# Kernel tuning notes

Measured on AMD Instinct MI355X. Metric: run time of the kernel, lower is better.

Reference implementation:

```python
import jax, jax.numpy as jnp
import numpy as np

B, N, D, S, ITERS = 64, 4096, 256, 8, 3
EPS = 1e-5


def _ln(x, g, b):
    m = jnp.mean(x, axis=-1, keepdims=True)
    v = jnp.mean((x - m) ** 2, axis=-1, keepdims=True)
    return (x - m) * jax.lax.rsqrt(v + EPS) * g + b


def setup_inputs() -> dict:
    key = jax.random.key(0)
    ks = jax.random.split(key, 20)
    s = 1.0 / np.sqrt(D)
    inp = {
        'x': jax.random.normal(ks[0], (B, N, D), jnp.float32),
        'noise': jax.random.normal(ks[1], (B, S, D), jnp.float32),
        'slot_mu': jax.random.normal(ks[2], (1, 1, D), jnp.float32),
        'slot_sigma': jax.random.normal(ks[3], (1, 1, D), jnp.float32) * 0.1,
        'Wq': jax.random.uniform(ks[4], (D, D), jnp.float32, -s, s),
        'bq': jnp.zeros((D,), jnp.float32),
        'Wk': jax.random.uniform(ks[5], (D, D), jnp.float32, -s, s),
        'bk': jnp.zeros((D,), jnp.float32),
        'Wv': jax.random.uniform(ks[6], (D, D), jnp.float32, -s, s),
        'bv': jnp.zeros((D,), jnp.float32),
        'W_ih': jax.random.uniform(ks[7], (3 * D, D), jnp.float32, -s, s),
        'b_ih': jnp.zeros((3 * D,), jnp.float32),
        'W_hh': jax.random.uniform(ks[8], (3 * D, D), jnp.float32, -s, s),
        'b_hh': jnp.zeros((3 * D,), jnp.float32),
        'W1': jax.random.uniform(ks[9], (D, D), jnp.float32, -s, s),
        'b1': jnp.zeros((D,), jnp.float32),
        'W2': jax.random.uniform(ks[10], (D, D), jnp.float32, -s, s),
        'b2': jnp.zeros((D,), jnp.float32),
        'g_in': jnp.ones((D,), jnp.float32), 'be_in': jnp.zeros((D,), jnp.float32),
        'g_sl': jnp.ones((D,), jnp.float32), 'be_sl': jnp.zeros((D,), jnp.float32),
        'g_mlp': jnp.ones((D,), jnp.float32), 'be_mlp': jnp.zeros((D,), jnp.float32),
    }
    return inp


def reference(x, noise, slot_mu, slot_sigma, Wq, bq, Wk, bk, Wv, bv,
              W_ih, b_ih, W_hh, b_hh, W1, b1, W2, b2,
              g_in, be_in, g_sl, be_sl, g_mlp, be_mlp):
    # slot init: mu + exp(sigma) * noise, broadcast over (B, S, D)
    slots = slot_mu + jnp.exp(slot_sigma) * noise

    xn = _ln(x, g_in, be_in)
    k = jnp.einsum('bnd,ed->bne', xn, Wk) + bk
    v = jnp.einsum('bnd,ed->bne', xn, Wv) + bv

    for _ in range(ITERS):
        sn = _ln(slots, g_sl, be_sl)
        q = jnp.einsum('bsd,ed->bse', sn, Wq) + bq
        attn_logits = jnp.einsum('bsd,bnd->bsn', q, k)
        attn = jax.nn.softmax(attn_logits, axis=-1)  # softmax over inputs N (as in source)
        updates = jnp.einsum('bnd,bsn->bsd', v, attn)

        # GRUCell: input=updates, hidden=slots (flattened over B*S)
        u = updates.reshape(-1, D)
        h = slots.reshape(-1, D)
        gx = u @ W_ih.T + b_ih
        gh = h @ W_hh.T + b_hh
        xr, xz, xn_g = jnp.split(gx, 3, axis=-1)
        hr, hz, hn_g = jnp.split(gh, 3, axis=-1)
        r = jax.nn.sigmoid(xr + hr)
        z = jax.nn.sigmoid(xz + hz)
        n = jnp.tanh(xn_g + r * hn_g)
        h = (1.0 - z) * n + z * h
        slots = h.reshape(x.shape[0], -1, D)

        m = _ln(slots, g_mlp, be_mlp)
        slots = slots + jax.nn.relu(m @ W1.T + b1) @ W2.T + b2
    return slots
```

## Files before the change

kernel.cpp:

```cpp
#include <hip/hip_runtime.h>

#define B_ 64
#define N_ 4096
#define D_ 256
#define S_ 8
#define EPSL 1e-5f

typedef _Float16 f16x8 __attribute__((ext_vector_type(8)));
typedef _Float16 f16x4 __attribute__((ext_vector_type(4)));
typedef float f32x4 __attribute__((ext_vector_type(4)));

__device__ __forceinline__ void gload_lds16_nt(const void* g, void* l){
    __builtin_amdgcn_global_load_lds(
        (const __attribute__((address_space(1))) unsigned int*)g,
        (__attribute__((address_space(3))) unsigned int*)l, 16, 0, 2);
}

__global__ __launch_bounds__(256) void k_ln_x(const float* __restrict__ x,
        const float* __restrict__ g, const float* __restrict__ be,
        _Float16* __restrict__ xn) {
    int w = threadIdx.x >> 6, l = threadIdx.x & 63;
    long row = (long)blockIdx.x * 4 + w;
    float4 xv = *(const float4*)(x + row * D_ + l * 4);
    float s = xv.x + xv.y + xv.z + xv.w;
    float q = xv.x*xv.x + xv.y*xv.y + xv.z*xv.z + xv.w*xv.w;
    #pragma unroll
    for (int m = 1; m < 64; m <<= 1) { s += __shfl_xor(s, m); q += __shfl_xor(q, m); }
    float mean = s * (1.0f/D_);
    float var = q * (1.0f/D_) - mean*mean;
    float inv = rsqrtf(var + EPSL);
    float4 gv = *(const float4*)(g + l*4);
    float4 bv = *(const float4*)(be + l*4);
    f16x4 o;
    o[0] = (_Float16)((xv.x-mean)*inv*gv.x + bv.x);
    o[1] = (_Float16)((xv.y-mean)*inv*gv.y + bv.y);
    o[2] = (_Float16)((xv.z-mean)*inv*gv.z + bv.z);
    o[3] = (_Float16)((xv.w-mean)*inv*gv.w + bv.w);
    *(f16x4*)(xn + row * D_ + l*4) = o;
}

__global__ __launch_bounds__(256) void k_wprep(const float* __restrict__ Whh,
        const float* __restrict__ W1, const float* __restrict__ W2,
        _Float16* __restrict__ Whhf, _Float16* __restrict__ W1f,
        _Float16* __restrict__ W2f) {
    int r = blockIdx.x, t = threadIdx.x;
    const float* src; _Float16* dst; int row;
    if (r < 768){ src = Whh; dst = Whhf; row = r; }
    else if (r < 1024){ src = W1; dst = W1f; row = r - 768; }
    else { src = W2; dst = W2f; row = r - 1024; }
    float v = src[(long)(r < 768 ? r : (r < 1024 ? r-768 : r-1024))*256 + t];
    long di = (long)((((row>>4)*8 + (t>>5))*64 + ((t>>3)&3)*16 + (row&15)))*8 + (t&7);
    dst[di] = (_Float16)v;
}

__global__ __launch_bounds__(256) void k_wprep2(const float* __restrict__ Wih,
        const float* __restrict__ Wv, const float* __restrict__ Wq,
        const float* __restrict__ Wk, const float* __restrict__ bih,
        const float* __restrict__ bv, const float* __restrict__ bq,
        _Float16* __restrict__ Wcf, _Float16* __restrict__ Wqkf,
        float* __restrict__ bc, float* __restrict__ cq) {
    __shared__ float a[4][256];
    int r = blockIdx.x, t = threadIdx.x;
    int w = t>>6, l = t&63;
    bool isC = (r < 192);
    if (isC){
        #pragma unroll
        for (int k=0;k<4;k++) a[k][t] = Wih[(long)(r*4+k)*256 + t];
    } else {
        int dbase = (r-192)*4;
        #pragma unroll
        for (int k=0;k<4;k++) a[k][t] = Wk[(long)t*256 + dbase + k];
    }
    __syncthreads();
    float ac[4] = {0.f,0.f,0.f,0.f};
    const float* Bm = isC ? Wv : Wq;
    for (int e=0;e<256;e++){
        float bvv = Bm[(long)e*256 + t];
        ac[0] += a[0][e]*bvv; ac[1] += a[1][e]*bvv;
        ac[2] += a[2][e]*bvv; ac[3] += a[3][e]*bvv;
    }
    _Float16* dst = isC ? Wcf : Wqkf;
    int rb = isC ? r*4 : (r-192)*4;
    #pragma unroll
    for (int k=0;k<4;k++){
        int row = rb + k;
        long di = (long)((((row>>4)*8 + (t>>5))*64 + ((t>>3)&3)*16 + (row&15)))*8 + (t&7);
        dst[di] = (_Float16)ac[k];
    }
    if (w < 4){
        const float* bvec = isC ? bv : bq;
        float p = 0.f;
        #pragma unroll
        for (int q=0;q<4;q++) p += a[w][l + q*64] * bvec[l + q*64];
        #pragma unroll
        for (int m=1;m<64;m<<=1) p += __shfl_xor(p, m);
        if (l==0){
            if (isC) bc[r*4 + w] = p + bih[r*4 + w];
            else     cq[(r-192)*4 + w] = p;
        }
    }
}

__device__ __forceinline__ void a16_st4(_Float16* a, int row, int col, float4 v){
    int byte = row*512 + ((col*2) ^ ((row&7)<<4));
    f16x4 h; h[0]=(_Float16)v.x; h[1]=(_Float16)v.y; h[2]=(_Float16)v.z; h[3]=(_Float16)v.w;
    *(f16x4*)((char*)a + byte) = h;
}
__device__ __forceinline__ void a16_st2(_Float16* a, int row, int col, _Float16 v){
    int byte = row*512 + ((col*2) ^ ((row&7)<<4));
    *(_Float16*)((char*)a + byte) = v;
}
__device__ __forceinline__ f16x8 a16_ld8(const _Float16* a, int row, int col){
    int byte = row*512 + ((col*2) ^ ((row&7)<<4));
    return *(const f16x8*)((const char*)a + byte);
}
__device__ __forceinline__ f16x8 wfrag_ld(const _Float16* __restrict__ Wf,
        int tt, int ks, int l){
    return *(const f16x8*)(Wf + ((long)tt*4096 + (ks*64 + l)*8));
}

template<int NT, int OS>
__device__ __forceinline__ void mm_stage_f(const _Float16* a16,
        const _Float16* __restrict__ Wf, float* outl, int w, int l){
    int lr = l&15, lh = l>>4;
    f16x8 A[8];
    #pragma unroll
    for (int ks=0;ks<8;ks++) A[ks] = a16_ld8(a16, lr, lh*8 + ks*32);
    #pragma unroll
    for (int tile=0; tile<NT; ++tile){
        int tt = w*NT + tile;
        f32x4 acc = {0.f,0.f,0.f,0.f};
        #pragma unroll
        for (int ks=0;ks<8;ks++)
            acc = __builtin_amdgcn_mfma_f32_16x16x32_f16(A[ks], wfrag_ld(Wf,tt,ks,l), acc, 0,0,0);
        if (lh < 2){
            #pragma unroll
            for (int r=0;r<4;r++) outl[(lh*4+r)*OS + tt*16 + lr] = acc[r];
        }
    }
}

__device__ __forceinline__ void mm_gates_f(const _Float16* au, const _Float16* ah,
        const _Float16* __restrict__ Wcf, const _Float16* __restrict__ Whf,
        float* g1, float* g2, int w, int l){
    int lr = l&15, lh = l>>4;
    f16x8 Au[8], Ah[8];
    #pragma unroll
    for (int ks=0;ks<8;ks++){ Au[ks] = a16_ld8(au, lr, lh*8+ks*32);
                              Ah[ks] = a16_ld8(ah, lr, lh*8+ks*32); }
    #pragma unroll
    for (int tile=0; tile<6; ++tile){
        int tt = w*6 + tile;
        f32x4 a1 = {0.f,0.f,0.f,0.f}, a2 = {0.f,0.f,0.f,0.f};
        #pragma unroll
        for (int ks=0;ks<8;ks++)
            a1 = __builtin_amdgcn_mfma_f32_16x16x32_f16(Au[ks], wfrag_ld(Wcf,tt,ks,l), a1, 0,0,0);
        #pragma unroll
        for (int ks=0;ks<8;ks++)
            a2 = __builtin_amdgcn_mfma_f32_16x16x32_f16(Ah[ks], wfrag_ld(Whf,tt,ks,l), a2, 0,0,0);
        if (lh < 2){
            #pragma unroll
            for (int r=0;r<4;r++){
                int s = lh*4+r;
                g1[s*768 + tt*16 + lr] = a1[r];
                g2[s*768 + tt*16 + lr] = a2[r];
            }
        }
    }
}

__global__ __launch_bounds__(512) void k_init(const float* __restrict__ noise,
        const float* __restrict__ mu, const float* __restrict__ sg,
        const float* __restrict__ g_sl, const float* __restrict__ be_sl,
        const _Float16* __restrict__ Wqkf, const float* __restrict__ cq,
        float* __restrict__ slots, _Float16* __restrict__ qh16) {
    __shared__ __align__(16) _Float16 a16[16*256];
    __shared__ float g1[8*256];
    int t = threadIdx.x, w = t>>6, l = t&63, b = blockIdx.x;
    int col = l*4;
    float4 nz = *(const float4*)(noise + ((long)b*8+w)*256 + col);
    float4 muv = *(const float4*)(mu + col);
    float4 sgv = *(const float4*)(sg + col);
    float4 sl;
    sl.x = muv.x + __expf(sgv.x)*nz.x; sl.y = muv.y + __expf(sgv.y)*nz.y;
    sl.z = muv.z + __expf(sgv.z)*nz.z; sl.w = muv.w + __expf(sgv.w)*nz.w;
    *(float4*)(slots + ((long)b*8+w)*256 + col) = sl;
    float s1 = sl.x+sl.y+sl.z+sl.w;
    float s2 = sl.x*sl.x+sl.y*sl.y+sl.z*sl.z+sl.w*sl.w;
    #pragma unroll
    for (int m=1;m<64;m<<=1){ s1+=__shfl_xor(s1,m); s2+=__shfl_xor(s2,m); }
    float mean = s1*(1.0f/D_);
    float inv = rsqrtf(s2*(1.0f/D_) - mean*mean + EPSL);
    float4 gv = *(const float4*)(g_sl + col);
    float4 bb = *(const float4*)(be_sl + col);
    float4 sn;
    sn.x=(sl.x-mean)*inv*gv.x+bb.x; sn.y=(sl.y-mean)*inv*gv.y+bb.y;
    sn.z=(sl.z-mean)*inv*gv.z+bb.z; sn.w=(sl.w-mean)*inv*gv.w+bb.w;
    a16_st4(a16, w, col, sn);
    float4 z = {0.f,0.f,0.f,0.f};
    a16_st4(a16, 8+w, col, z);
    __syncthreads();
    mm_stage_f<2,256>(a16, Wqkf, g1, w, l);
    __syncthreads();
    for (int idx=t; idx<2048; idx+=512){
        int s = idx>>8, d = idx&255;
        qh16[((long)b*16+s)*D_ + d] = (_Float16)(g1[s*256+d] + cq[d]);
        qh16[((long)b*16+8+s)*D_ + d] = (_Float16)0.f;
    }
}

__global__ __launch_bounds__(256) void k_attn(const _Float16* __restrict__ xn,
        const _Float16* __restrict__ qh16,
        _Float16* __restrict__ pacc, float* __restrict__ ppsum,
        float* __restrict__ pmax) {
    __shared__ __align__(16) char xt_raw[4*16384];
    __shared__ __align__(16) float pt_s[4][16][8];
    __shared__ float mw_s[4][8], psw_s[4][8];
    int t = threadIdx.x, w = t>>6, l = t&63, lr = l&15, lh = l>>4;
    int c = blockIdx.x, b = blockIdx.y;

    f16x8 A[8];
    const _Float16* qbase = qh16 + ((long)b*16 + lr)*D_ + lh*8;
    #pragma unroll
    for (int ks=0;ks<8;ks++) A[ks] = *(const f16x8*)(qbase + ks*32);
    asm volatile("s_waitcnt vmcnt(0)" ::: "memory");

    char* xw = xt_raw + w*16384;
    const char* xnb = (const char*)(xn + (long)b*N_*D_);
    int rlo = l>>5;
    int cb  = (l&31)*16;

    {
        int n0 = c*512 + w*16;
        #pragma unroll
        for (int j=0;j<8;j++){
            int row = 2*j + rlo;
            const char* gp = xnb + (long)(n0+row)*512 + (cb ^ ((row&7)<<4));
            gload_lds16_nt(gp, xw + j*1024);
        }
    }

    float m8[8];
    #pragma unroll
    for (int s=0;s<8;s++) m8[s] = -1e30f;
    float acc[8][4] = {};
    float psr[4] = {0.f,0.f,0.f,0.f};
    float (*pt)[8] = pt_s[w];
    int fx = (lr&7)<<4;

    for (int sc=0; sc<8; ++sc){
        const char* curb = xw + ((sc&1)<<13);
        char* nxtb = xw + (((sc+1)&1)<<13);
        if (sc < 7){
            asm volatile("s_waitcnt lgkmcnt(0)" ::: "memory");
            int n0n = c*512 + (sc+1)*64 + w*16;
            #pragma unroll
            for (int j=0;j<8;j++){
                int row = 2*j + rlo;
                const char* gp = xnb + (long)(n0n+row)*512 + (cb ^ ((row&7)<<4));
                gload_lds16_nt(gp, nxtb + j*1024);
            }
            asm volatile("s_waitcnt vmcnt(8)" ::: "memory");
        } else {
            asm volatile("s_waitcnt vmcnt(0)" ::: "memory");
        }
        __builtin_amdgcn_sched_barrier(0);

        f32x4 lacc = {0.f,0.f,0.f,0.f};
        #pragma unroll
        for (int ks=0;ks<8;ks++){
            f16x8 Bf = *(const f16x8*)(curb + lr*512 + ((lh*16 + ks*64) ^ fx));
            lacc = __builtin_amdgcn_mfma_f32_16x16x32_f16(A[ks], Bf, lacc, 0,0,0);
        }
        float tm[4];
        #pragma unroll
        for (int r=0;r<4;r++) tm[r] = lacc[r];
        #pragma unroll
        for (int m=1;m<16;m<<=1){
            #pragma unroll
            for (int r=0;r<4;r++) tm[r] = fmaxf(tm[r], __shfl_xor(tm[r], m));
        }
        float mN[8];
        #pragma unroll
        for (int r=0;r<4;r++){ mN[r] = __shfl(tm[r], lr); mN[4+r] = __shfl(tm[r], 16+lr); }
        float sc8[8];
        #pragma unroll
        for (int s=0;s<8;s++){
            float mn = fmaxf(m8[s], mN[s]);
            sc8[s] = __expf(m8[s] - mn);
            m8[s] = mn;
        }
        #pragma unroll
        for (int s=0;s<8;s++){
            acc[s][0]*=sc8[s]; acc[s][1]*=sc8[s]; acc[s][2]*=sc8[s]; acc[s][3]*=sc8[s];
        }
        if (lh < 2){
            float4 pv;
            #pragma unroll
            for (int r=0;r<4;r++){
                int s = lh*4+r;
                float p = __expf(lacc[r] - m8[s]);
                psr[r] = psr[r]*sc8[s] + p;
                ((float*)&pv)[r] = p;
            }
            *(float4*)&pt[lr][lh*4] = pv;
        }
        #pragma unroll 4
        for (int i=0;i<16;i++){
            float4 p0 = *(const float4*)&pt[i][0];
            float4 p1 = *(const float4*)&pt[i][4];
            f16x4 xv = *(const f16x4*)(curb + i*512 + ((l*8) ^ ((i&7)<<4)));
            float x0=(float)xv[0], x1=(float)xv[1], x2=(float)xv[2], x3=(float)xv[3];
            acc[0][0]+=p0.x*x0; acc[0][1]+=p0.x*x1; acc[0][2]+=p0.x*x2; acc[0][3]+=p0.x*x3;
            acc[1][0]+=p0.y*x0; acc[1][1]+=p0.y*x1; acc[1][2]+=p0.y*x2; acc[1][3]+=p0.y*x3;
            acc[2][0]+=p0.z*x0; acc[2][1]+=p0.z*x1; acc[2][2]+=p0.z*x2; acc[2][3]+=p0.z*x3;
            acc[3][0]+=p0.w*x0; acc[3][1]+=p0.w*x1; acc[3][2]+=p0.w*x2; acc[3][3]+=p0.w*x3;
            acc[4][0]+=p1.x*x0; acc[4][1]+=p1.x*x1; acc[4][2]+=p1.x*x2; acc[4][3]+=p1.x*x3;
            acc[5][0]+=p1.y*x0; acc[5][1]+=p1.y*x1; acc[5][2]+=p1.y*x2; acc[5][3]+=p1.y*x3;
            acc[6][0]+=p1.z*x0; acc[6][1]+=p1.z*x1; acc[6][2]+=p1.z*x2; acc[6][3]+=p1.z*x3;
            acc[7][0]+=p1.w*x0; acc[7][1]+=p1.w*x1; acc[7][2]+=p1.w*x2; acc[7][3]+=p1.w*x3;
        }
    }
    #pragma unroll
    for (int m=1;m<16;m<<=1){
        #pragma unroll
        for (int r=0;r<4;r++) psr[r] += __shfl_xor(psr[r], m);
    }
    if (l == 0){
        #pragma unroll
        for (int s=0;s<8;s++) mw_s[w][s] = m8[s];
        #pragma unroll
        for (int r=0;r<4;r++) psw_s[w][r] = psr[r];
    }
    if (l == 16){
        #pragma unroll
        for (int r=0;r<4;r++) psw_s[w][4+r] = psr[r];
    }
    __syncthreads();
    float M8[8];
    #pragma unroll
    for (int s=0;s<8;s++)
        M8[s] = fmaxf(fmaxf(mw_s[0][s],mw_s[1][s]), fmaxf(mw_s[2][s],mw_s[3][s]));
    float* accw = (float*)xt_raw;
    #pragma unroll
    for (int s=0;s<8;s++){
        float wsc = __expf(m8[s] - M8[s]);
        float4 v;
        v.x=acc[s][0]*wsc; v.y=acc[s][1]*wsc; v.z=acc[s][2]*wsc; v.w=acc[s][3]*wsc;
        *(float4*)&accw[((w*8+s)<<8) + l*4] = v;
    }
    __syncthreads();
    for (int pair=t; pair<2048; pair+=256){
        int s = pair>>8, d = pair&255;
        float v = accw[(s<<8)+d] + accw[((8+s)<<8)+d] + accw[((16+s)<<8)+d] + accw[((24+s)<<8)+d];
        pacc[(((long)b*8 + c)*8 + s)*D_ + d] = (_Float16)v;
    }
    if (t < 8){
        float ps = 0.f;
        #pragma unroll
        for (int w2=0;w2<4;w2++) ps += __expf(mw_s[w2][t]-M8[t]) * psw_s[w2][t];
        ppsum[((long)b*8+c)*8 + t] = ps;
        pmax [((long)b*8+c)*8 + t] = M8[t];
    }
}

__global__ __launch_bounds__(512) void k_tail(
    const _Float16* __restrict__ pacc, const float* __restrict__ ppsum,
    const float* __restrict__ pmax, const float* __restrict__ slots,
    const _Float16* __restrict__ Wcf, const float* __restrict__ bc,
    const _Float16* __restrict__ Whhf, const float* __restrict__ bhh,
    const _Float16* __restrict__ W1f, const float* __restrict__ b1,
    const _Float16* __restrict__ W2f, const float* __restrict__ b2,
    const float* __restrict__ gm, const float* __restrict__ bem,
    const float* __restrict__ g_sl, const float* __restrict__ be_sl,
    const _Float16* __restrict__ Wqkf, const float* __restrict__ cq,
    float* __restrict__ out, _Float16* __restrict__ qh16, int last) {
    int t = threadIdx.x, w = t>>6, l = t&63;
    int b = blockIdx.x;
    __shared__ float hb[8][256], hn[8][256];
    __shared__ float g1[8*768], g2[8*768];
    __shared__ __align__(16) _Float16 a16a[16*256], a16b[16*256];
    __shared__ float pss[8];
    __shared__ float wcs[8][8];

    if (t < 8){
        float pm[8]; float M = -1e30f;
        #pragma unroll
        for (int c=0;c<8;c++){ pm[c] = pmax[((long)b*8+c)*8+t]; M = fmaxf(M, pm[c]); }
        float ps = 0.f;
        #pragma unroll
        for (int c=0;c<8;c++){
            float wc = __expf(pm[c]-M);
            wcs[t][c] = wc;
            ps += wc*ppsum[((long)b*8+c)*8+t];
        }
        pss[t] = ps;
    }
    __syncthreads();
    for (int idx=t; idx<2048; idx+=512){
        int s = idx>>8, d = idx&255;
        float v = 0.f;
        #pragma unroll
        for (int c=0;c<8;c++) v += wcs[s][c]*(float)pacc[(((long)b*8+c)*8+s)*D_ + d];
        float axv = v / pss[s];
        float hbv = slots[((long)b*8+s)*D_ + d];
        hb[s][d] = hbv;
        a16_st2(a16a, s, d, (_Float16)axv);
        a16_st2(a16b, s, d, (_Float16)hbv);
    }
    {   float4 z = {0.f,0.f,0.f,0.f};
        a16_st4(a16a, 8+w, l*4, z);
        a16_st4(a16b, 8+w, l*4, z);
    }
    __syncthreads();
    mm_gates_f(a16a, a16b, Wcf, Whhf, g1, g2, w, l);
    __syncthreads();
    {
        int d0 = l*4;
        float hn4[4];
        #pragma unroll
        for (int i=0;i<4;i++){
            int d = d0+i;
            float r = 1.f/(1.f+__expf(-(g1[w*768+d]     + bc[d]     + g2[w*768+d]     + bhh[d])));
            float z = 1.f/(1.f+__expf(-(g1[w*768+256+d] + bc[256+d] + g2[w*768+256+d] + bhh[256+d])));
            float gg = g1[w*768+512+d] + bc[512+d] + r*(g2[w*768+512+d] + bhh[512+d]);
            float e2 = __expf(2.f*gg);
            float nn = 1.f - 2.f/(e2+1.f);
            hn4[i] = (1.f-z)*nn + z*hb[w][d];
            hn[w][d] = hn4[i];
        }
        float s1 = hn4[0]+hn4[1]+hn4[2]+hn4[3];
        float s2 = hn4[0]*hn4[0]+hn4[1]*hn4[1]+hn4[2]*hn4[2]+hn4[3]*hn4[3];
        #pragma unroll
        for (int m=1;m<64;m<<=1){ s1+=__shfl_xor(s1,m); s2+=__shfl_xor(s2,m); }
        float mean = s1*(1.0f/D_);
        float inv = rsqrtf(s2*(1.0f/D_) - mean*mean + EPSL);
        float4 gv = *(const float4*)(gm + d0);
        float4 bb = *(const float4*)(bem + d0);
        float4 v;
        v.x=(hn4[0]-mean)*inv*gv.x+bb.x; v.y=(hn4[1]-mean)*inv*gv.y+bb.y;
        v.z=(hn4[2]-mean)*inv*gv.z+bb.z; v.w=(hn4[3]-mean)*inv*gv.w+bb.w;
        a16_st4(a16a, w, d0, v);
    }
    __syncthreads();
    mm_stage_f<2,256>(a16a, W1f, g1, w, l);
    __syncthreads();
    {
        int d0 = l*4;
        float4 v = *(const float4*)&g1[w*256+d0];
        float4 bb = *(const float4*)(b1 + d0);
        v.x=fmaxf(v.x+bb.x,0.f); v.y=fmaxf(v.y+bb.y,0.f);
        v.z=fmaxf(v.z+bb.z,0.f); v.w=fmaxf(v.w+bb.w,0.f);
        a16_st4(a16b, w, d0, v);
    }
    __syncthreads();
    mm_stage_f<2,256>(a16b, W2f, g2, w, l);
    __syncthreads();
    {
        int d0 = l*4;
        float4 bb = *(const float4*)(b2 + d0);
        float4 o4;
        o4.x = hn[w][d0]   + g2[w*256+d0]   + bb.x;
        o4.y = hn[w][d0+1] + g2[w*256+d0+1] + bb.y;
        o4.z = hn[w][d0+2] + g2[w*256+d0+2] + bb.z;
        o4.w = hn[w][d0+3] + g2[w*256+d0+3] + bb.w;
        *(float4*)(out + ((long)b*8+w)*D_ + d0) = o4;
        if (!last){
            float s1 = o4.x+o4.y+o4.z+o4.w;
            float s2 = o4.x*o4.x+o4.y*o4.y+o4.z*o4.z+o4.w*o4.w;
            #pragma unroll
            for (int m=1;m<64;m<<=1){ s1+=__shfl_xor(s1,m); s2+=__shfl_xor(s2,m); }
            float mean = s1*(1.0f/D_);
            float inv = rsqrtf(s2*(1.0f/D_) - mean*mean + EPSL);
            float4 gv = *(const float4*)(g_sl + d0);
            float4 be = *(const float4*)(be_sl + d0);
            float4 v;
            v.x=(o4.x-mean)*inv*gv.x+be.x; v.y=(o4.y-mean)*inv*gv.y+be.y;
            v.z=(o4.z-mean)*inv*gv.z+be.z; v.w=(o4.w-mean)*inv*gv.w+be.w;
            a16_st4(a16a, w, d0, v);
        }
    }
    if (last) return;
    __syncthreads();
    mm_stage_f<2,256>(a16a, Wqkf, g1, w, l);
    __syncthreads();
    for (int idx=t; idx<2048; idx+=512){
        int s = idx>>8, d = idx&255;
        qh16[((long)b*16+s)*D_ + d] = (_Float16)(g1[s*256+d] + cq[d]);
    }
}

extern "C" void kernel_launch(void* const* d_in, const int* in_sizes, int n_in,
                              void* d_out, int out_size, void* d_ws, size_t ws_size,
                              hipStream_t stream) {
    const float* x     = (const float*)d_in[0];
    const float* noise = (const float*)d_in[1];
    const float* mu    = (const float*)d_in[2];
    const float* sg    = (const float*)d_in[3];
    const float* Wq    = (const float*)d_in[4];
    const float* bq    = (const float*)d_in[5];
    const float* Wk    = (const float*)d_in[6];
    const float* Wv    = (const float*)d_in[8];
    const float* bv    = (const float*)d_in[9];
    const float* Wih   = (const float*)d_in[10];
    const float* bih   = (const float*)d_in[11];
    const float* Whh   = (const float*)d_in[12];
    const float* bhh   = (const float*)d_in[13];
    const float* W1    = (const float*)d_in[14];
    const float* b1    = (const float*)d_in[15];
    const float* W2    = (const float*)d_in[16];
    const float* b2    = (const float*)d_in[17];
    const float* g_in  = (const float*)d_in[18];
    const float* be_in = (const float*)d_in[19];
    const float* g_sl  = (const float*)d_in[20];
    const float* be_sl = (const float*)d_in[21];
    const float* g_mlp = (const float*)d_in[22];
    const float* be_mlp= (const float*)d_in[23];

    char* ws = (char*)d_ws;
    _Float16* xn16  = (_Float16*)(ws);
    _Float16* qh16  = (_Float16*)(ws + 134217728);
    float*    slots = (float*)   (ws + 134742016);
    _Float16* pacc  = (_Float16*)(ws + 135266304);
    float*    ppsum = (float*)   (ws + 152043520);
    float*    pmax  = (float*)   (ws + 152059904);
    _Float16* w16f  = (_Float16*)(ws + 152076288);
    float*    bc    = (float*)   (ws + 153255936);
    float*    cq    = (float*)   (ws + 153259008);

    _Float16* Wcf  = w16f;
    _Float16* Whhf = w16f + 196608;
    _Float16* W1f  = w16f + 393216;
    _Float16* W2f  = w16f + 458752;
    _Float16* Wqkf = w16f + 524288;

    hipLaunchKernelGGL(k_wprep, dim3(1280), dim3(256), 0, stream,
                       Whh, W1, W2, Whhf, W1f, W2f);
    hipLaunchKernelGGL(k_wprep2, dim3(256), dim3(256), 0, stream,
                       Wih, Wv, Wq, Wk, bih, bv, bq, Wcf, Wqkf, bc, cq);
    hipLaunchKernelGGL(k_ln_x, dim3(65536), dim3(256), 0, stream, x, g_in, be_in, xn16);
    hipLaunchKernelGGL(k_init, dim3(64), dim3(512), 0, stream,
                       noise, mu, sg, g_sl, be_sl, Wqkf, cq, slots, qh16);
    for (int it = 0; it < 3; it++){
        hipLaunchKernelGGL(k_attn, dim3(8,64), dim3(256), 0, stream,
                           xn16, qh16, pacc, ppsum, pmax);
        float* dst = (it==2) ? (float*)d_out : slots;
        hipLaunchKernelGGL(k_tail, dim3(64), dim3(512), 0, stream,
                           pacc, ppsum, pmax, slots,
                           Wcf, bc, Whhf, bhh, W1f, b1, W2f, b2,
                           g_mlp, be_mlp, g_sl, be_sl, Wqkf, cq,
                           dst, qh16, (it==2) ? 1 : 0);
    }
}
```

Measured before the change: 265.0 us.

## Fuse preprocessing kernels into one launch with direct fp32 initial query

Merges the weight-prep, input layernorm and slot-init kernels into a single grid whose block ranges each run one of the former jobs, cutting three launches and their serialization. Because k_init depended on Wqkf from k_wprep2, the initial query is now computed directly in fp32 by applying Wq then Wk per slot row in scalar loops, so there is no dependency inside the launch. This removes the ordering hazard, but the scalar per-slot matvecs are slower per block than the former MFMA path and the rounding differs slightly from the fused Wqk path.

```diff
diff --git a/kernel.cpp b/kernel.cpp
--- a/kernel.cpp
+++ b/kernel.cpp
@@ -16,91 +16,6 @@
         (__attribute__((address_space(3))) unsigned int*)l, 16, 0, 2);
 }
 
-__global__ __launch_bounds__(256) void k_ln_x(const float* __restrict__ x,
-        const float* __restrict__ g, const float* __restrict__ be,
-        _Float16* __restrict__ xn) {
-    int w = threadIdx.x >> 6, l = threadIdx.x & 63;
-    long row = (long)blockIdx.x * 4 + w;
-    float4 xv = *(const float4*)(x + row * D_ + l * 4);
-    float s = xv.x + xv.y + xv.z + xv.w;
-    float q = xv.x*xv.x + xv.y*xv.y + xv.z*xv.z + xv.w*xv.w;
-    #pragma unroll
-    for (int m = 1; m < 64; m <<= 1) { s += __shfl_xor(s, m); q += __shfl_xor(q, m); }
-    float mean = s * (1.0f/D_);
-    float var = q * (1.0f/D_) - mean*mean;
-    float inv = rsqrtf(var + EPSL);
-    float4 gv = *(const float4*)(g + l*4);
-    float4 bv = *(const float4*)(be + l*4);
-    f16x4 o;
-    o[0] = (_Float16)((xv.x-mean)*inv*gv.x + bv.x);
-    o[1] = (_Float16)((xv.y-mean)*inv*gv.y + bv.y);
-    o[2] = (_Float16)((xv.z-mean)*inv*gv.z + bv.z);
-    o[3] = (_Float16)((xv.w-mean)*inv*gv.w + bv.w);
-    *(f16x4*)(xn + row * D_ + l*4) = o;
-}
-
-__global__ __launch_bounds__(256) void k_wprep(const float* __restrict__ Whh,
-        const float* __restrict__ W1, const float* __restrict__ W2,
-        _Float16* __restrict__ Whhf, _Float16* __restrict__ W1f,
-        _Float16* __restrict__ W2f) {
-    int r = blockIdx.x, t = threadIdx.x;
-    const float* src; _Float16* dst; int row;
-    if (r < 768){ src = Whh; dst = Whhf; row = r; }
-    else if (r < 1024){ src = W1; dst = W1f; row = r - 768; }
-    else { src = W2; dst = W2f; row = r - 1024; }
-    float v = src[(long)(r < 768 ? r : (r < 1024 ? r-768 : r-1024))*256 + t];
-    long di = (long)((((row>>4)*8 + (t>>5))*64 + ((t>>3)&3)*16 + (row&15)))*8 + (t&7);
-    dst[di] = (_Float16)v;
-}
-
-__global__ __launch_bounds__(256) void k_wprep2(const float* __restrict__ Wih,
-        const float* __restrict__ Wv, const float* __restrict__ Wq,
-        const float* __restrict__ Wk, const float* __restrict__ bih,
-        const float* __restrict__ bv, const float* __restrict__ bq,
-        _Float16* __restrict__ Wcf, _Float16* __restrict__ Wqkf,
-        float* __restrict__ bc, float* __restrict__ cq) {
-    __shared__ float a[4][256];
-    int r = blockIdx.x, t = threadIdx.x;
-    int w = t>>6, l = t&63;
-    bool isC = (r < 192);
-    if (isC){
-        #pragma unroll
-        for (int k=0;k<4;k++) a[k][t] = Wih[(long)(r*4+k)*256 + t];
-    } else {
-        int dbase = (r-192)*4;
-        #pragma unroll
-        for (int k=0;k<4;k++) a[k][t] = Wk[(long)t*256 + dbase + k];
-    }
-    __syncthreads();
-    float ac[4] = {0.f,0.f,0.f,0.f};
-    const float* Bm = isC ? Wv : Wq;
-    for (int e=0;e<256;e++){
-        float bvv = Bm[(long)e*256 + t];
-        ac[0] += a[0][e]*bvv; ac[1] += a[1][e]*bvv;
-        ac[2] += a[2][e]*bvv; ac[3] += a[3][e]*bvv;
-    }
-    _Float16* dst = isC ? Wcf : Wqkf;
-    int rb = isC ? r*4 : (r-192)*4;
-    #pragma unroll
-    for (int k=0;k<4;k++){
-        int row = rb + k;
-        long di = (long)((((row>>4)*8 + (t>>5))*64 + ((t>>3)&3)*16 + (row&15)))*8 + (t&7);
-        dst[di] = (_Float16)ac[k];
-    }
-    if (w < 4){
-        const float* bvec = isC ? bv : bq;
-        float p = 0.f;
-        #pragma unroll
-        for (int q=0;q<4;q++) p += a[w][l + q*64] * bvec[l + q*64];
-        #pragma unroll
-        for (int m=1;m<64;m<<=1) p += __shfl_xor(p, m);
-        if (l==0){
-            if (isC) bc[r*4 + w] = p + bih[r*4 + w];
-            else     cq[(r-192)*4 + w] = p;
-        }
-    }
-}
-
 __device__ __forceinline__ void a16_st4(_Float16* a, int row, int col, float4 v){
     int byte = row*512 + ((col*2) ^ ((row&7)<<4));
     f16x4 h; h[0]=(_Float16)v.x; h[1]=(_Float16)v.y; h[2]=(_Float16)v.z; h[3]=(_Float16)v.w;
@@ -119,93 +34,128 @@
     return *(const f16x8*)(Wf + ((long)tt*4096 + (ks*64 + l)*8));
 }
 
-template<int NT, int OS>
-__device__ __forceinline__ void mm_stage_f(const _Float16* a16,
-        const _Float16* __restrict__ Wf, float* outl, int w, int l){
-    int lr = l&15, lh = l>>4;
-    f16x8 A[8];
-    #pragma unroll
-    for (int ks=0;ks<8;ks++) A[ks] = a16_ld8(a16, lr, lh*8 + ks*32);
-    #pragma unroll
-    for (int tile=0; tile<NT; ++tile){
-        int tt = w*NT + tile;
-        f32x4 acc = {0.f,0.f,0.f,0.f};
-        #pragma unroll
-        for (int ks=0;ks<8;ks++)
-            acc = __builtin_amdgcn_mfma_f32_16x16x32_f16(A[ks], wfrag_ld(Wf,tt,ks,l), acc, 0,0,0);
-        if (lh < 2){
-            #pragma unroll
-            for (int r=0;r<4;r++) outl[(lh*4+r)*OS + tt*16 + lr] = acc[r];
-        }
-    }
-}
-
-__device__ __forceinline__ void mm_gates_f(const _Float16* au, const _Float16* ah,
-        const _Float16* __restrict__ Wcf, const _Float16* __restrict__ Whf,
-        float* g1, float* g2, int w, int l){
-    int lr = l&15, lh = l>>4;
-    f16x8 Au[8], Ah[8];
-    #pragma unroll
-    for (int ks=0;ks<8;ks++){ Au[ks] = a16_ld8(au, lr, lh*8+ks*32);
-                              Ah[ks] = a16_ld8(ah, lr, lh*8+ks*32); }
-    #pragma unroll
-    for (int tile=0; tile<6; ++tile){
-        int tt = w*6 + tile;
-        f32x4 a1 = {0.f,0.f,0.f,0.f}, a2 = {0.f,0.f,0.f,0.f};
-        #pragma unroll
-        for (int ks=0;ks<8;ks++)
-            a1 = __builtin_amdgcn_mfma_f32_16x16x32_f16(Au[ks], wfrag_ld(Wcf,tt,ks,l), a1, 0,0,0);
-        #pragma unroll
-        for (int ks=0;ks<8;ks++)
-            a2 = __builtin_amdgcn_mfma_f32_16x16x32_f16(Ah[ks], wfrag_ld(Whf,tt,ks,l), a2, 0,0,0);
-        if (lh < 2){
-            #pragma unroll
-            for (int r=0;r<4;r++){
-                int s = lh*4+r;
-                g1[s*768 + tt*16 + lr] = a1[r];
-                g2[s*768 + tt*16 + lr] = a2[r];
+__global__ __launch_bounds__(256) void k_pre(
+        const float* __restrict__ x, const float* __restrict__ g_in,
+        const float* __restrict__ be_in, _Float16* __restrict__ xn,
+        const float* __restrict__ Whh, const float* __restrict__ W1,
+        const float* __restrict__ W2, _Float16* __restrict__ Whhf,
+        _Float16* __restrict__ W1f, _Float16* __restrict__ W2f,
+        const float* __restrict__ Wih, const float* __restrict__ Wv,
+        const float* __restrict__ Wq, const float* __restrict__ Wk,
+        const float* __restrict__ bih, const float* __restrict__ bv,
+        const float* __restrict__ bq, _Float16* __restrict__ Wcf,
+        _Float16* __restrict__ Wqkf, float* __restrict__ bc,
+        float* __restrict__ cq,
+        const float* __restrict__ noise, const float* __restrict__ mu,
+        const float* __restrict__ sg, const float* __restrict__ g_sl,
+        const float* __restrict__ be_sl, float* __restrict__ slots,
+        _Float16* __restrict__ qh16) {
+    __shared__ float a4[4][256];
+    __shared__ float sn[256], ql[256], red[10];
+    int r = blockIdx.x, t = threadIdx.x;
+    int w = t>>6, l = t&63;
+    if (r >= 2048){
+        long row = (long)(r - 2048) * 4 + w;
+        float4 xv = *(const float4*)(x + row * D_ + l * 4);
+        float s = xv.x + xv.y + xv.z + xv.w;
+        float q = xv.x*xv.x + xv.y*xv.y + xv.z*xv.z + xv.w*xv.w;
+        #pragma unroll
+        for (int m = 1; m < 64; m <<= 1) { s += __shfl_xor(s, m); q += __shfl_xor(q, m); }
+        float mean = s * (1.0f/D_);
+        float inv = rsqrtf(q * (1.0f/D_) - mean*mean + EPSL);
+        float4 gv = *(const float4*)(g_in + l*4);
+        float4 bb = *(const float4*)(be_in + l*4);
+        f16x4 o;
+        o[0] = (_Float16)((xv.x-mean)*inv*gv.x + bb.x);
+        o[1] = (_Float16)((xv.y-mean)*inv*gv.y + bb.y);
+        o[2] = (_Float16)((xv.z-mean)*inv*gv.z + bb.z);
+        o[3] = (_Float16)((xv.w-mean)*inv*gv.w + bb.w);
+        *(f16x4*)(xn + row * D_ + l*4) = o;
+        return;
+    }
+    if (r < 512){
+        int b = r>>3, s8 = r&7;
+        long base = (long)(b*8+s8) * D_;
+        float v = mu[t] + __expf(sg[t]) * noise[base + t];
+        slots[base + t] = v;
+        float s = v, q = v*v;
+        #pragma unroll
+        for (int m=1;m<64;m<<=1){ s+=__shfl_xor(s,m); q+=__shfl_xor(q,m);}
+        if (l==0){ red[w]=s; red[4+w]=q; }
+        __syncthreads();
+        if (t==0){
+            float ss=red[0]+red[1]+red[2]+red[3];
+            float qq=red[4]+red[5]+red[6]+red[7];
+            float mean = ss*(1.0f/D_);
+            red[8]=mean; red[9]=rsqrtf(qq*(1.0f/D_) - mean*mean + EPSL);
+        }
+        __syncthreads();
+        float mean=red[8], inv=red[9];
+        sn[t] = (v-mean)*inv*g_sl[t] + be_sl[t];
+        __syncthreads();
+        float acc = bq[t];
+        const float4* wr = (const float4*)(Wq + (long)t*D_);
+        const float4* sv = (const float4*)sn;
+        for (int e=0;e<64;e++){ float4 a=wr[e], b4=sv[e];
+            acc += a.x*b4.x + a.y*b4.y + a.z*b4.z + a.w*b4.w; }
+        ql[t]=acc;
+        __syncthreads();
+        float qh=0.f;
+        for (int e=0;e<D_;e++) qh += ql[e]*Wk[(long)e*D_ + t];
+        qh16[((long)b*16 + s8)*D_ + t] = (_Float16)qh;
+        qh16[((long)b*16 + 8 + s8)*D_ + t] = (_Float16)0.f;
+        return;
+    }
+    if (r < 768){
+        int rr = r - 512;
+        bool isC = (rr < 192);
+        if (isC){
+            #pragma unroll
+            for (int k=0;k<4;k++) a4[k][t] = Wih[(long)(rr*4+k)*256 + t];
+        } else {
+            int dbase = (rr-192)*4;
+            #pragma unroll
+            for (int k=0;k<4;k++) a4[k][t] = Wk[(long)t*256 + dbase + k];
+        }
+        __syncthreads();
+        float ac[4] = {0.f,0.f,0.f,0.f};
+        const float* Bm = isC ? Wv : Wq;
+        for (int e=0;e<256;e++){
+            float bvv = Bm[(long)e*256 + t];
+            ac[0] += a4[0][e]*bvv; ac[1] += a4[1][e]*bvv;
+            ac[2] += a4[2][e]*bvv; ac[3] += a4[3][e]*bvv;
+        }
+        _Float16* dst = isC ? Wcf : Wqkf;
+        int rb = isC ? rr*4 : (rr-192)*4;
+        #pragma unroll
+        for (int k=0;k<4;k++){
+            int row = rb + k;
+            long di = (long)((((row>>4)*8 + (t>>5))*64 + ((t>>3)&3)*16 + (row&15)))*8 + (t&7);
+            dst[di] = (_Float16)ac[k];
+        }
+        if (w < 4){
+            const float* bvec = isC ? bv : bq;
+            float p = 0.f;
+            #pragma unroll
+            for (int q=0;q<4;q++) p += a4[w][l + q*64] * bvec[l + q*64];
+            #pragma unroll
+            for (int m=1;m<64;m<<=1) p += __shfl_xor(p, m);
+            if (l==0){
+                if (isC) bc[rr*4 + w] = p + bih[rr*4 + w];
+                else     cq[(rr-192)*4 + w] = p;
             }
         }
-    }
-}
-
-__global__ __launch_bounds__(512) void k_init(const float* __restrict__ noise,
-        const float* __restrict__ mu, const float* __restrict__ sg,
-        const float* __restrict__ g_sl, const float* __restrict__ be_sl,
-        const _Float16* __restrict__ Wqkf, const float* __restrict__ cq,
-        float* __restrict__ slots, _Float16* __restrict__ qh16) {
-    __shared__ __align__(16) _Float16 a16[16*256];
-    __shared__ float g1[8*256];
-    int t = threadIdx.x, w = t>>6, l = t&63, b = blockIdx.x;
-    int col = l*4;
-    float4 nz = *(const float4*)(noise + ((long)b*8+w)*256 + col);
-    float4 muv = *(const float4*)(mu + col);
-    float4 sgv = *(const float4*)(sg + col);
-    float4 sl;
-    sl.x = muv.x + __expf(sgv.x)*nz.x; sl.y = muv.y + __expf(sgv.y)*nz.y;
-    sl.z = muv.z + __expf(sgv.z)*nz.z; sl.w = muv.w + __expf(sgv.w)*nz.w;
-    *(float4*)(slots + ((long)b*8+w)*256 + col) = sl;
-    float s1 = sl.x+sl.y+sl.z+sl.w;
-    float s2 = sl.x*sl.x+sl.y*sl.y+sl.z*sl.z+sl.w*sl.w;
-    #pragma unroll
-    for (int m=1;m<64;m<<=1){ s1+=__shfl_xor(s1,m); s2+=__shfl_xor(s2,m); }
-    float mean = s1*(1.0f/D_);
-    float inv = rsqrtf(s2*(1.0f/D_) - mean*mean + EPSL);
-    float4 gv = *(const float4*)(g_sl + col);
-    float4 bb = *(const float4*)(be_sl + col);
-    float4 sn;
-    sn.x=(sl.x-mean)*inv*gv.x+bb.x; sn.y=(sl.y-mean)*inv*gv.y+bb.y;
-    sn.z=(sl.z-mean)*inv*gv.z+bb.z; sn.w=(sl.w-mean)*inv*gv.w+bb.w;
-    a16_st4(a16, w, col, sn);
-    float4 z = {0.f,0.f,0.f,0.f};
-    a16_st4(a16, 8+w, col, z);
-    __syncthreads();
-    mm_stage_f<2,256>(a16, Wqkf, g1, w, l);
-    __syncthreads();
-    for (int idx=t; idx<2048; idx+=512){
-        int s = idx>>8, d = idx&255;
-        qh16[((long)b*16+s)*D_ + d] = (_Float16)(g1[s*256+d] + cq[d]);
-        qh16[((long)b*16+8+s)*D_ + d] = (_Float16)0.f;
+        return;
+    }
+    {
+        int rr = r - 768;
+        const float* src; _Float16* dst; int row;
+        if (rr < 768){ src = Whh; dst = Whhf; row = rr; }
+        else if (rr < 1024){ src = W1; dst = W1f; row = rr - 768; }
+        else { src = W2; dst = W2f; row = rr - 1024; }
+        float v = src[(long)row*256 + t];
+        long di = (long)((((row>>4)*8 + (t>>5))*64 + ((t>>3)&3)*16 + (row&15)))*8 + (t&7);
+        dst[di] = (_Float16)v;
     }
 }
 
@@ -230,8 +180,7 @@
     int rlo = l>>5;
     int cb  = (l&31)*16;
 
-    {
-        int n0 = c*512 + w*16;
+    {   int n0 = c*512 + w*16;
         #pragma unroll
         for (int j=0;j<8;j++){
             int row = 2*j + rlo;
@@ -361,6 +310,56 @@
         for (int w2=0;w2<4;w2++) ps += __expf(mw_s[w2][t]-M8[t]) * psw_s[w2][t];
         ppsum[((long)b*8+c)*8 + t] = ps;
         pmax [((long)b*8+c)*8 + t] = M8[t];
+    }
+}
+
+template<int NT, int OS>
+__device__ __forceinline__ void mm_stage_f(const _Float16* a16,
+        const _Float16* __restrict__ Wf, float* outl, int w, int l){
+    int lr = l&15, lh = l>>4;
+    f16x8 A[8];
+    #pragma unroll
+    for (int ks=0;ks<8;ks++) A[ks] = a16_ld8(a16, lr, lh*8 + ks*32);
+    #pragma unroll
+    for (int tile=0; tile<NT; ++tile){
+        int tt = w*NT + tile;
+        f32x4 acc = {0.f,0.f,0.f,0.f};
+        #pragma unroll
+        for (int ks=0;ks<8;ks++)
+            acc = __builtin_amdgcn_mfma_f32_16x16x32_f16(A[ks], wfrag_ld(Wf,tt,ks,l), acc, 0,0,0);
+        if (lh < 2){
+            #pragma unroll
+            for (int r=0;r<4;r++) outl[(lh*4+r)*OS + tt*16 + lr] = acc[r];
+        }
+    }
+}
+
+__device__ __forceinline__ void mm_gates_f(const _Float16* au, const _Float16* ah,
+        const _Float16* __restrict__ Wcf, const _Float16* __restrict__ Whf,
+        float* g1, float* g2, int w, int l){
+    int lr = l&15, lh = l>>4;
+    f16x8 Au[8], Ah[8];
+    #pragma unroll
+    for (int ks=0;ks<8;ks++){ Au[ks] = a16_ld8(au, lr, lh*8+ks*32);
+                              Ah[ks] = a16_ld8(ah, lr, lh*8+ks*32); }
+    #pragma unroll
+    for (int tile=0; tile<6; ++tile){
+        int tt = w*6 + tile;
+        f32x4 a1 = {0.f,0.f,0.f,0.f}, a2 = {0.f,0.f,0.f,0.f};
+        #pragma unroll
+        for (int ks=0;ks<8;ks++)
+            a1 = __builtin_amdgcn_mfma_f32_16x16x32_f16(Au[ks], wfrag_ld(Wcf,tt,ks,l), a1, 0,0,0);
+        #pragma unroll
+        for (int ks=0;ks<8;ks++)
+            a2 = __builtin_amdgcn_mfma_f32_16x16x32_f16(Ah[ks], wfrag_ld(Whf,tt,ks,l), a2, 0,0,0);
+        if (lh < 2){
+            #pragma unroll
+            for (int r=0;r<4;r++){
+                int s = lh*4+r;
+                g1[s*768 + tt*16 + lr] = a1[r];
+                g2[s*768 + tt*16 + lr] = a2[r];
+            }
+        }
     }
 }
 
@@ -534,13 +533,11 @@
     _Float16* W2f  = w16f + 458752;
     _Float16* Wqkf = w16f + 524288;
 
-    hipLaunchKernelGGL(k_wprep, dim3(1280), dim3(256), 0, stream,
-                       Whh, W1, W2, Whhf, W1f, W2f);
-    hipLaunchKernelGGL(k_wprep2, dim3(256), dim3(256), 0, stream,
-                       Wih, Wv, Wq, Wk, bih, bv, bq, Wcf, Wqkf, bc, cq);
-    hipLaunchKernelGGL(k_ln_x, dim3(65536), dim3(256), 0, stream, x, g_in, be_in, xn16);
-    hipLaunchKernelGGL(k_init, dim3(64), dim3(512), 0, stream,
-                       noise, mu, sg, g_sl, be_sl, Wqkf, cq, slots, qh16);
+    hipLaunchKernelGGL(k_pre, dim3(67584), dim3(256), 0, stream,
+                       x, g_in, be_in, xn16,
+                       Whh, W1, W2, Whhf, W1f, W2f,
+                       Wih, Wv, Wq, Wk, bih, bv, bq, Wcf, Wqkf, bc, cq,
+                       noise, mu, sg, g_sl, be_sl, slots, qh16);
     for (int it = 0; it < 3; it++){
         hipLaunchKernelGGL(k_attn, dim3(8,64), dim3(256), 0, stream,
                            xn16, qh16, pacc, ppsum, pmax);
```

Measured after the change: 284.6 us. 7.4% more time.
